# Kernel tuning notes

Hardware: AMD Instinct MI355X
Metric: run time of the kernel (lower is better)

The kernel has to match this reference:

```python
import jax, jax.numpy as jnp
import numpy as np

N = 100000   # nodes
E = 1600000  # edges (avg degree 16)
F_IN = 64
H = 64
C = 40       # classes


def setup_inputs() -> dict:
    key = jax.random.key(0)
    ks = jax.random.split(key, 12)

    def lin(k, out_d, in_d):
        kw, kb = jax.random.split(k)
        W = jax.random.normal(kw, (out_d, in_d), jnp.float32) / jnp.sqrt(jnp.float32(in_d))
        b = jnp.zeros((out_d,), jnp.float32)
        return W, b

    Wl1, b1 = lin(ks[2], H, F_IN)
    Wr1, _ = lin(ks[3], H, F_IN)
    Wl2, b2 = lin(ks[4], H, H)
    Wr2, _ = lin(ks[5], H, H)
    Wl3, b3 = lin(ks[6], C, H)
    Wr3, _ = lin(ks[7], C, H)

    return {
        "x": jax.random.normal(ks[0], (N, F_IN), jnp.float32),
        "edge_index": jax.random.randint(ks[1], (2, E), 0, N, jnp.int32),
        "Wl1": Wl1, "Wr1": Wr1, "b1": b1,
        "Wl2": Wl2, "Wr2": Wr2, "b2": b2,
        "Wl3": Wl3, "Wr3": Wr3, "b3": b3,
    }


def _sage_conv(x, src, dst, Wl, Wr, b, n_nodes):
    # PyG SAGEConv (aggr='mean'): out = lin_l(mean_{j in N(i)} x_j) + lin_r(x_i)
    msg = x[src]                                                   # [E, F] gather
    agg_sum = jax.ops.segment_sum(msg, dst, num_segments=n_nodes)  # [N, F]
    deg = jax.ops.segment_sum(jnp.ones((src.shape[0],), x.dtype), dst,
                              num_segments=n_nodes)                # [N]
    agg = agg_sum / jnp.maximum(deg, 1.0)[:, None]                 # mean aggregation
    return agg @ Wl.T + b + x @ Wr.T


def reference(x, edge_index, Wl1, Wr1, b1, Wl2, Wr2, b2, Wl3, Wr3, b3):
    src, dst = edge_index[0], edge_index[1]
    n = x.shape[0]
    # dropout is identity in eval mode (training=self.training)
    h = jax.nn.relu(_sage_conv(x, src, dst, Wl1, Wr1, b1, n))
    h = jax.nn.relu(_sage_conv(h, src, dst, Wl2, Wr2, b2, n))
    h = _sage_conv(h, src, dst, Wl3, Wr3, b3, n)
    return jax.nn.log_softmax(h, axis=1)
```

## Files before the change

### kernel.cpp

```cpp
#include <hip/hip_runtime.h>
#include <hip/hip_bf16.h>
#include <math.h>


#define BK_SHIFT 7
#define BK_NODES 128
#define NB_MAX   1024

typedef __attribute__((ext_vector_type(8))) short short8;
typedef __attribute__((ext_vector_type(4))) float f32x4;

__device__ inline float blo(unsigned v) { union { unsigned u; float f; } c; c.u = v << 16; return c.f; }
__device__ inline float bhi(unsigned v) { union { unsigned u; float f; } c; c.u = v & 0xFFFF0000u; return c.f; }
__device__ inline unsigned short f2bf(float f) {
    union { float f; unsigned u; } c; c.f = f;
    unsigned r = (c.u + 0x7FFFu + ((c.u >> 16) & 1u)) >> 16;
    return (unsigned short)r;
}

__global__ __launch_bounds__(256) void prep_kernel(const int* __restrict__ dstA, int* __restrict__ bcount,
                                                   int E, int NB,
                                                   const float* __restrict__ x, unsigned short* __restrict__ Xb, int n8,
                                                   const float* __restrict__ Wl1, const float* __restrict__ Wr1,
                                                   const float* __restrict__ Wl2, const float* __restrict__ Wr2,
                                                   const float* __restrict__ Wl3, const float* __restrict__ Wr3,
                                                   unsigned short* __restrict__ Wb1,
                                                   unsigned short* __restrict__ Wb2,
                                                   unsigned short* __restrict__ Wb3) {
    int b = blockIdx.x, t = threadIdx.x;
    if (b < 256) {
        __shared__ int lc[NB_MAX];
        for (int i = t; i < NB; i += 256) lc[i] = 0;
        __syncthreads();
        for (int e = b * 256 + t; e < E; e += 256 * 256)
            atomicAdd(&lc[dstA[e] >> BK_SHIFT], 1);
        __syncthreads();
        for (int i = t; i < NB; i += 256)
            if (lc[i]) atomicAdd(&bcount[i], lc[i]);
    } else if (b < 344) {
        int i = (b - 256) * 256 + t;
        if (i < 8192) {
            int c = i >> 7, k = i & 127;
            float v = (k < 64) ? Wl1[c * 64 + k] : Wr1[c * 64 + k - 64];
            Wb1[i] = f2bf(v);
        } else if (i < 16384) {
            int j = i - 8192;
            int c = j >> 7, k = j & 127;
            float v = (k < 64) ? Wl2[c * 64 + k] : Wr2[c * 64 + k - 64];
            Wb2[j] = f2bf(v);
        } else if (i < 22528) {
            int j = i - 16384;
            int c = j >> 6, k = j & 63;
            float v = 0.f;
            if (c < 40) v = Wl3[c * 64 + k];
            else if (c >= 48 && c < 88) v = Wr3[(c - 48) * 64 + k];
            Wb3[j] = f2bf(v);
        }
    } else {
        for (int i = (b - 344) * 256 + t; i < n8; i += 1024 * 256) {
            const float* p = x + (size_t)i * 8;
            float4 a = *(const float4*)p;
            float4 bq = *(const float4*)(p + 4);
            uint4 o;
            o.x = f2bf(a.x) | ((unsigned)f2bf(a.y) << 16);
            o.y = f2bf(a.z) | ((unsigned)f2bf(a.w) << 16);
            o.z = f2bf(bq.x) | ((unsigned)f2bf(bq.y) << 16);
            o.w = f2bf(bq.z) | ((unsigned)f2bf(bq.w) << 16);
            *(uint4*)(Xb + (size_t)i * 8) = o;
        }
    }
}

__global__ __launch_bounds__(1024) void bscan_kernel(const int* __restrict__ bcount,
                                                     int* __restrict__ bbase,
                                                     int* __restrict__ cursor, int NB, int E) {
    __shared__ int s[1024];
    int t = threadIdx.x;
    int v = (t < NB) ? bcount[t] : 0;
    s[t] = v;
    __syncthreads();
    for (int off = 1; off < 1024; off <<= 1) {
        int x = 0;
        if (t >= off) x = s[t - off];
        __syncthreads();
        s[t] += x;
        __syncthreads();
    }
    if (t < NB) {
        int ex = s[t] - v;
        bbase[t] = ex;
        cursor[t] = ex;
    }
    if (t == 0) bbase[NB] = E;
}

__global__ __launch_bounds__(256) void bin_kernel(const int* __restrict__ srcA,
                                                  const int* __restrict__ dstA,
                                                  int* __restrict__ cursor,
                                                  int* __restrict__ binned, int E, int NB) {
    __shared__ int lc[NB_MAX];
    __shared__ int lbase[NB_MAX];
    int t = threadIdx.x;
    int chunk = (E + gridDim.x - 1) / gridDim.x;
    int e0 = blockIdx.x * chunk;
    int e1 = min(E, e0 + chunk);
    for (int i = t; i < NB; i += 256) lc[i] = 0;
    __syncthreads();
    for (int e = e0 + t; e < e1; e += 256)
        atomicAdd(&lc[dstA[e] >> BK_SHIFT], 1);
    __syncthreads();
    for (int i = t; i < NB; i += 256) {
        int c = lc[i];
        lbase[i] = c ? atomicAdd(&cursor[i], c) : 0;
    }
    __syncthreads();
    for (int i = t; i < NB; i += 256) lc[i] = 0;
    __syncthreads();
    for (int e = e0 + t; e < e1; e += 256) {
        int d = dstA[e];
        int b = d >> BK_SHIFT;
        int r = atomicAdd(&lc[b], 1);
        binned[lbase[b] + r] = srcA[e] | ((d & (BK_NODES - 1)) << 24);
    }
}

__global__ __launch_bounds__(256) void bsort_kernel(const int* __restrict__ binned,
                                                    const int* __restrict__ bbase,
                                                    int* __restrict__ col,
                                                    int* __restrict__ row_start, int N) {
    __shared__ int cnt[BK_NODES];
    __shared__ int base[BK_NODES];
    __shared__ int s[BK_NODES];
    int b = blockIdx.x, t = threadIdx.x;
    int e0 = bbase[b], e1 = bbase[b + 1];
    if (t < BK_NODES) cnt[t] = 0;
    __syncthreads();
    for (int e = e0 + t; e < e1; e += 256)
        atomicAdd(&cnt[(unsigned)binned[e] >> 24], 1);
    __syncthreads();
    int v = (t < BK_NODES) ? cnt[t] : 0;
    if (t < BK_NODES) s[t] = v;
    __syncthreads();
    for (int off = 1; off < BK_NODES; off <<= 1) {
        int x = 0;
        if (t < BK_NODES && t >= off) x = s[t - off];
        __syncthreads();
        if (t < BK_NODES) s[t] += x;
        __syncthreads();
    }
    if (t < BK_NODES) {
        base[t] = e0 + s[t] - v;
        int node = b * BK_NODES + t;
        if (node < N) row_start[node] = base[t];
        cnt[t] = 0;
    }
    if (b == gridDim.x - 1 && t == 0) row_start[N] = e1;
    __syncthreads();
    for (int e = e0 + t; e < e1; e += 256) {
        unsigned p = (unsigned)binned[e];
        int dl = p >> 24;
        int pos = base[dl] + atomicAdd(&cnt[dl], 1);
        col[pos] = p & 0xFFFFFF;
    }
}

__global__ __launch_bounds__(256) void agg64_kernel(const unsigned short* __restrict__ X,
                                                    const int* __restrict__ rs,
                                                    const int* __restrict__ col,
                                                    unsigned short* __restrict__ OUT, int n) {
    int t = threadIdx.x;
    int node = blockIdx.x * 32 + (t >> 3);
    if (node >= n) return;
    int lane = t & 7;
    int s = rs[node], d = rs[node + 1] - s;
    const unsigned short* lp = X + lane * 8;
    float a0 = 0.f, a1 = 0.f, a2 = 0.f, a3 = 0.f, a4 = 0.f, a5 = 0.f, a6 = 0.f, a7 = 0.f;
    int j = 0;
    for (; j + 3 < d; j += 4) {
        int c0 = col[s + j], c1 = col[s + j + 1];
        int c2 = col[s + j + 2], c3 = col[s + j + 3];
        uint4 q0 = *(const uint4*)(lp + (size_t)c0 * 64);
        uint4 q1 = *(const uint4*)(lp + (size_t)c1 * 64);
        uint4 q2 = *(const uint4*)(lp + (size_t)c2 * 64);
        uint4 q3 = *(const uint4*)(lp + (size_t)c3 * 64);
        a0 += (blo(q0.x) + blo(q1.x)) + (blo(q2.x) + blo(q3.x));
        a1 += (bhi(q0.x) + bhi(q1.x)) + (bhi(q2.x) + bhi(q3.x));
        a2 += (blo(q0.y) + blo(q1.y)) + (blo(q2.y) + blo(q3.y));
        a3 += (bhi(q0.y) + bhi(q1.y)) + (bhi(q2.y) + bhi(q3.y));
        a4 += (blo(q0.z) + blo(q1.z)) + (blo(q2.z) + blo(q3.z));
        a5 += (bhi(q0.z) + bhi(q1.z)) + (bhi(q2.z) + bhi(q3.z));
        a6 += (blo(q0.w) + blo(q1.w)) + (blo(q2.w) + blo(q3.w));
        a7 += (bhi(q0.w) + bhi(q1.w)) + (bhi(q2.w) + bhi(q3.w));
    }
    for (; j < d; ++j) {
        int c0 = col[s + j];
        uint4 q0 = *(const uint4*)(lp + (size_t)c0 * 64);
        a0 += blo(q0.x); a1 += bhi(q0.x); a2 += blo(q0.y); a3 += bhi(q0.y);
        a4 += blo(q0.z); a5 += bhi(q0.z); a6 += blo(q0.w); a7 += bhi(q0.w);
    }
    float w = 1.f / (float)(d > 0 ? d : 1);
    a0 *= w; a1 *= w; a2 *= w; a3 *= w; a4 *= w; a5 *= w; a6 *= w; a7 *= w;
    uint4 o;
    o.x = f2bf(a0) | ((unsigned)f2bf(a1) << 16);
    o.y = f2bf(a2) | ((unsigned)f2bf(a3) << 16);
    o.z = f2bf(a4) | ((unsigned)f2bf(a5) << 16);
    o.w = f2bf(a6) | ((unsigned)f2bf(a7) << 16);
    *(uint4*)(OUT + (size_t)node * 64 + lane * 8) = o;
}

__global__ __launch_bounds__(256) void linmfma12_kernel(const unsigned short* __restrict__ A,
                                                        const unsigned short* __restrict__ X,
                                                        const unsigned short* __restrict__ Wb,
                                                        const float* __restrict__ bias,
                                                        unsigned short* __restrict__ OUT,
                                                        int N) {
    __shared__ unsigned short Ys[64][136];
    __shared__ unsigned short Ws[64][136];
    int t = threadIdx.x;
    int rowbase = blockIdx.x * 64;
#pragma unroll
    for (int it = 0; it < 4; ++it) {
        int idx = it * 256 + t;
        int row = idx >> 4, c = idx & 15;
        int grow = rowbase + row;
        if (grow >= N) grow = N - 1;
        const unsigned short* src = (c < 8) ? (A + (size_t)grow * 64 + c * 8)
                                            : (X + (size_t)grow * 64 + (c - 8) * 8);
        *(short8*)&Ys[row][c * 8] = *(const short8*)src;
        *(short8*)&Ws[row][c * 8] = *(const short8*)(Wb + (size_t)row * 128 + c * 8);
    }
    __syncthreads();
    int l = t & 63, w = t >> 6;
    int lrow = l & 15, lk = l >> 4;
    f32x4 acc0 = {0.f, 0.f, 0.f, 0.f};
    f32x4 acc1 = acc0, acc2 = acc0, acc3 = acc0;
#pragma unroll
    for (int kk = 0; kk < 4; ++kk) {
        int ko = kk * 32 + lk * 8;
        short8 a  = *(const short8*)&Ys[16 * w + lrow][ko];
        short8 b0 = *(const short8*)&Ws[lrow][ko];
        short8 b1 = *(const short8*)&Ws[16 + lrow][ko];
        short8 b2 = *(const short8*)&Ws[32 + lrow][ko];
        short8 b3 = *(const short8*)&Ws[48 + lrow][ko];
        acc0 = __builtin_amdgcn_mfma_f32_16x16x32_bf16(a, b0, acc0, 0, 0, 0);
        acc1 = __builtin_amdgcn_mfma_f32_16x16x32_bf16(a, b1, acc1, 0, 0, 0);
        acc2 = __builtin_amdgcn_mfma_f32_16x16x32_bf16(a, b2, acc2, 0, 0, 0);
        acc3 = __builtin_amdgcn_mfma_f32_16x16x32_bf16(a, b3, acc3, 0, 0, 0);
    }
#define EPI12(nt, accv)                                                   \
    {                                                                     \
        int colc = 16 * (nt) + lrow;                                      \
        float bv = bias[colc];                                            \
        _Pragma("unroll") for (int i = 0; i < 4; ++i) {                   \
            int grow = rowbase + 16 * w + lk * 4 + i;                     \
            if (grow < N) {                                               \
                float v = fmaxf(accv[i] + bv, 0.f);                       \
                OUT[(size_t)grow * 64 + colc] = f2bf(v);                  \
            }                                                             \
        }                                                                 \
    }
    EPI12(0, acc0) EPI12(1, acc1) EPI12(2, acc2) EPI12(3, acc3)
#undef EPI12
}

__global__ __launch_bounds__(256) void linmfma3_kernel(const unsigned short* __restrict__ H,
                                                       const unsigned short* __restrict__ Wb3,
                                                       const float* __restrict__ b3,
                                                       unsigned short* __restrict__ Z,
                                                       float* __restrict__ R,
                                                       int N) {
    __shared__ unsigned short Ys[64][72];
    __shared__ unsigned short Ws[96][72];
    int t = threadIdx.x;
    int rowbase = blockIdx.x * 64;
#pragma unroll
    for (int it = 0; it < 2; ++it) {
        int idx = it * 256 + t;
        int row = idx >> 3, c = idx & 7;
        int grow = rowbase + row;
        if (grow >= N) grow = N - 1;
        *(short8*)&Ys[row][c * 8] = *(const short8*)(H + (size_t)grow * 64 + c * 8);
    }
#pragma unroll
    for (int it = 0; it < 3; ++it) {
        int idx = it * 256 + t;
        int row = idx >> 3, c = idx & 7;
        *(short8*)&Ws[row][c * 8] = *(const short8*)(Wb3 + (size_t)row * 64 + c * 8);
    }
    __syncthreads();
    int l = t & 63, w = t >> 6;
    int lrow = l & 15, lk = l >> 4;
    f32x4 acc0 = {0.f, 0.f, 0.f, 0.f};
    f32x4 acc1 = acc0, acc2 = acc0, acc3 = acc0, acc4 = acc0, acc5 = acc0;
#pragma unroll
    for (int kk = 0; kk < 2; ++kk) {
        int ko = kk * 32 + lk * 8;
        short8 a  = *(const short8*)&Ys[16 * w + lrow][ko];
        short8 b0 = *(const short8*)&Ws[lrow][ko];
        short8 b1 = *(const short8*)&Ws[16 + lrow][ko];
        short8 b2 = *(const short8*)&Ws[32 + lrow][ko];
        short8 b3f = *(const short8*)&Ws[48 + lrow][ko];
        short8 b4 = *(const short8*)&Ws[64 + lrow][ko];
        short8 b5 = *(const short8*)&Ws[80 + lrow][ko];
        acc0 = __builtin_amdgcn_mfma_f32_16x16x32_bf16(a, b0, acc0, 0, 0, 0);
        acc1 = __builtin_amdgcn_mfma_f32_16x16x32_bf16(a, b1, acc1, 0, 0, 0);
        acc2 = __builtin_amdgcn_mfma_f32_16x16x32_bf16(a, b2, acc2, 0, 0, 0);
        acc3 = __builtin_amdgcn_mfma_f32_16x16x32_bf16(a, b3f, acc3, 0, 0, 0);
        acc4 = __builtin_amdgcn_mfma_f32_16x16x32_bf16(a, b4, acc4, 0, 0, 0);
        acc5 = __builtin_amdgcn_mfma_f32_16x16x32_bf16(a, b5, acc5, 0, 0, 0);
    }
#define EPI3(nt, accv)                                                     \
    {                                                                      \
        int colc = 16 * (nt) + lrow;                                       \
        _Pragma("unroll") for (int i = 0; i < 4; ++i) {                    \
            int grow = rowbase + 16 * w + lk * 4 + i;                      \
            if (grow < N) {                                                \
                float v = accv[i];                                         \
                if (colc < 40) {                                           \
                    Z[(size_t)grow * 40 + colc] = f2bf(v);                 \
                } else if (colc >= 48 && colc < 88) {                      \
                    R[(size_t)grow * 40 + (colc - 48)] = v + b3[colc - 48];\
                }                                                          \
            }                                                              \
        }                                                                  \
    }
    EPI3(0, acc0) EPI3(1, acc1) EPI3(2, acc2) EPI3(3, acc3) EPI3(4, acc4) EPI3(5, acc5)
#undef EPI3
}

__global__ __launch_bounds__(256) void agg40lsm_kernel(const unsigned short* __restrict__ Z,
                                                       const int* __restrict__ rs,
                                                       const int* __restrict__ col,
                                                       float* __restrict__ out, int n) {
    int t = threadIdx.x;
    int node = blockIdx.x * 32 + (t >> 3);
    if (node >= n) return;
    int lane = t & 7;
    bool act = lane < 5;
    int s = rs[node], d = rs[node + 1] - s;
    const unsigned short* lp = Z + lane * 8;
    float a0 = 0.f, a1 = 0.f, a2 = 0.f, a3 = 0.f, a4 = 0.f, a5 = 0.f, a6 = 0.f, a7 = 0.f;
    int j = 0;
    for (; j + 3 < d; j += 4) {
        int c0 = col[s + j], c1 = col[s + j + 1];
        int c2 = col[s + j + 2], c3 = col[s + j + 3];
        if (act) {
            uint4 q0 = *(const uint4*)(lp + (size_t)c0 * 40);
            uint4 q1 = *(const uint4*)(lp + (size_t)c1 * 40);
            uint4 q2 = *(const uint4*)(lp + (size_t)c2 * 40);
            uint4 q3 = *(const uint4*)(lp + (size_t)c3 * 40);
            a0 += (blo(q0.x) + blo(q1.x)) + (blo(q2.x) + blo(q3.x));
            a1 += (bhi(q0.x) + bhi(q1.x)) + (bhi(q2.x) + bhi(q3.x));
            a2 += (blo(q0.y) + blo(q1.y)) + (blo(q2.y) + blo(q3.y));
            a3 += (bhi(q0.y) + bhi(q1.y)) + (bhi(q2.y) + bhi(q3.y));
            a4 += (blo(q0.z) + blo(q1.z)) + (blo(q2.z) + blo(q3.z));
            a5 += (bhi(q0.z) + bhi(q1.z)) + (bhi(q2.z) + bhi(q3.z));
            a6 += (blo(q0.w) + blo(q1.w)) + (blo(q2.w) + blo(q3.w));
            a7 += (bhi(q0.w) + bhi(q1.w)) + (bhi(q2.w) + bhi(q3.w));
        }
    }
    for (; j < d; ++j) {
        int c0 = col[s + j];
        if (act) {
            uint4 q0 = *(const uint4*)(lp + (size_t)c0 * 40);
            a0 += blo(q0.x); a1 += bhi(q0.x); a2 += blo(q0.y); a3 += bhi(q0.y);
            a4 += blo(q0.z); a5 += bhi(q0.z); a6 += blo(q0.w); a7 += bhi(q0.w);
        }
    }
    float w = 1.f / (float)(d > 0 ? d : 1);
    if (act) {
        float* op = out + (size_t)node * 40 + lane * 8;
        float4 r0 = *(const float4*)op;
        float4 r1 = *(const float4*)(op + 4);
        a0 = a0 * w + r0.x; a1 = a1 * w + r0.y; a2 = a2 * w + r0.z; a3 = a3 * w + r0.w;
        a4 = a4 * w + r1.x; a5 = a5 * w + r1.y; a6 = a6 * w + r1.z; a7 = a7 * w + r1.w;
    }
    float mx = act ? fmaxf(fmaxf(fmaxf(a0, a1), fmaxf(a2, a3)),
                           fmaxf(fmaxf(a4, a5), fmaxf(a6, a7))) : -3.4e38f;
#pragma unroll
    for (int off = 1; off < 8; off <<= 1) mx = fmaxf(mx, __shfl_xor(mx, off, 8));
    float ssum = act ? (expf(a0 - mx) + expf(a1 - mx) + expf(a2 - mx) + expf(a3 - mx) +
                        expf(a4 - mx) + expf(a5 - mx) + expf(a6 - mx) + expf(a7 - mx)) : 0.f;
#pragma unroll
    for (int off = 1; off < 8; off <<= 1) ssum += __shfl_xor(ssum, off, 8);
    float lg = mx + logf(ssum);
    if (act) {
        float* op = out + (size_t)node * 40 + lane * 8;
        float4 o0, o1;
        o0.x = a0 - lg; o0.y = a1 - lg; o0.z = a2 - lg; o0.w = a3 - lg;
        o1.x = a4 - lg; o1.y = a5 - lg; o1.z = a6 - lg; o1.w = a7 - lg;
        *(float4*)op = o0;
        *(float4*)(op + 4) = o1;
    }
}

extern "C" void kernel_launch(void* const* d_in, const int* in_sizes, int n_in,
                              void* d_out, int out_size, void* d_ws, size_t ws_size,
                              hipStream_t stream) {
    const float* x   = (const float*)d_in[0];
    const int*   ei  = (const int*)d_in[1];
    const float* Wl1 = (const float*)d_in[2];
    const float* Wr1 = (const float*)d_in[3];
    const float* b1  = (const float*)d_in[4];
    const float* Wl2 = (const float*)d_in[5];
    const float* Wr2 = (const float*)d_in[6];
    const float* b2  = (const float*)d_in[7];
    const float* Wl3 = (const float*)d_in[8];
    const float* Wr3 = (const float*)d_in[9];
    const float* b3  = (const float*)d_in[10];
    float* out = (float*)d_out;

    const int N = in_sizes[0] / 64;
    const int E = in_sizes[1] / 2;
    const int NB = (N + BK_NODES - 1) / BK_NODES;
    const int* srcA = ei;
    const int* dstA = ei + E;

    char* ws = (char*)d_ws;
    size_t off = 0;
    auto alloc = [&](size_t bytes) {
        off = (off + 255) & ~(size_t)255;
        char* p = ws + off;
        off += bytes;
        return p;
    };
    int* bcount    = (int*)alloc((size_t)(NB_MAX + 1) * 4);
    int* bbase     = (int*)alloc((size_t)(NB_MAX + 1) * 4);
    int* cursor    = (int*)alloc((size_t)NB_MAX * 4);
    int* binned    = (int*)alloc((size_t)E * 4);
    int* col       = (int*)alloc((size_t)E * 4);
    int* row_start = (int*)alloc((size_t)(N + 1) * 4);
    unsigned short* Xb  = (unsigned short*)alloc((size_t)N * 64 * 2);
    unsigned short* AGG = (unsigned short*)alloc((size_t)N * 64 * 2);
    unsigned short* Hb  = (unsigned short*)alloc((size_t)N * 64 * 2);
    unsigned short* Zb  = (unsigned short*)alloc((size_t)N * 40 * 2);
    unsigned short* Wb1 = (unsigned short*)alloc(8192 * 2);
    unsigned short* Wb2 = (unsigned short*)alloc(8192 * 2);
    unsigned short* Wb3 = (unsigned short*)alloc(6144 * 2);

    hipMemsetAsync(bcount, 0, (size_t)(NB + 1) * 4, stream);
    prep_kernel<<<1368, 256, 0, stream>>>(dstA, bcount, E, NB, x, Xb, N * 64 / 8,
                                          Wl1, Wr1, Wl2, Wr2, Wl3, Wr3, Wb1, Wb2, Wb3);
    bscan_kernel<<<1, 1024, 0, stream>>>(bcount, bbase, cursor, NB, E);
    bin_kernel<<<512, 256, 0, stream>>>(srcA, dstA, cursor, binned, E, NB);
    bsort_kernel<<<NB, 256, 0, stream>>>(binned, bbase, col, row_start, N);

    int gridA = (N + 31) / 32;
    int gridM = (N + 63) / 64;

    agg64_kernel<<<gridA, 256, 0, stream>>>(Xb, row_start, col, AGG, N);
    linmfma12_kernel<<<gridM, 256, 0, stream>>>(AGG, Xb, Wb1, b1, Hb, N);

    agg64_kernel<<<gridA, 256, 0, stream>>>(Hb, row_start, col, AGG, N);
    linmfma12_kernel<<<gridM, 256, 0, stream>>>(AGG, Hb, Wb2, b2, Hb, N);

    linmfma3_kernel<<<gridM, 256, 0, stream>>>(Hb, Wb3, b3, Zb, out, N);
    agg40lsm_kernel<<<gridA, 256, 0, stream>>>(Zb, row_start, col, out, N);
}
```

Measured before the change: 285.0 us.

## Replace atomic cursor binning with per-block count matrix and column scan

The prep kernel now writes a per-block, per-bucket histogram matrix instead of atomically accumulating global bucket counts. A new column-scan kernel computes each block's exclusive offset per bucket. The bin kernel then scatters directly without re-counting or using global atomics. This removes the bin kernel's second pass over the destinations, the global cursor atomics and the memset, at the cost of an extra kernel launch and about 2 MB of count/prefix traffic.

```diff
diff --git a/kernel.cpp b/kernel.cpp
--- a/kernel.cpp
+++ b/kernel.cpp
@@ -6,6 +6,7 @@
 #define BK_SHIFT 7
 #define BK_NODES 128
 #define NB_MAX   1024
+#define BBLK     256
 
 typedef __attribute__((ext_vector_type(8))) short short8;
 typedef __attribute__((ext_vector_type(4))) float f32x4;
@@ -18,7 +19,7 @@
     return (unsigned short)r;
 }
 
-__global__ __launch_bounds__(256) void prep_kernel(const int* __restrict__ dstA, int* __restrict__ bcount,
+__global__ __launch_bounds__(256) void prep_kernel(const int* __restrict__ dstA, int* __restrict__ cnts,
                                                    int E, int NB,
                                                    const float* __restrict__ x, unsigned short* __restrict__ Xb, int n8,
                                                    const float* __restrict__ Wl1, const float* __restrict__ Wr1,
@@ -28,17 +29,18 @@
                                                    unsigned short* __restrict__ Wb2,
                                                    unsigned short* __restrict__ Wb3) {
     int b = blockIdx.x, t = threadIdx.x;
-    if (b < 256) {
+    if (b < BBLK) {
         __shared__ int lc[NB_MAX];
-        for (int i = t; i < NB; i += 256) lc[i] = 0;
-        __syncthreads();
-        for (int e = b * 256 + t; e < E; e += 256 * 256)
+        for (int i = t; i < NB_MAX; i += 256) lc[i] = 0;
+        __syncthreads();
+        int chunk = (E + BBLK - 1) / BBLK;
+        int e0 = b * chunk, e1 = min(E, e0 + chunk);
+        for (int e = e0 + t; e < e1; e += 256)
             atomicAdd(&lc[dstA[e] >> BK_SHIFT], 1);
         __syncthreads();
-        for (int i = t; i < NB; i += 256)
-            if (lc[i]) atomicAdd(&bcount[i], lc[i]);
-    } else if (b < 344) {
-        int i = (b - 256) * 256 + t;
+        for (int i = t; i < NB_MAX; i += 256) cnts[b * NB_MAX + i] = lc[i];
+    } else if (b < BBLK + 88) {
+        int i = (b - BBLK) * 256 + t;
         if (i < 8192) {
             int c = i >> 7, k = i & 127;
             float v = (k < 64) ? Wl1[c * 64 + k] : Wr1[c * 64 + k - 64];
@@ -57,7 +59,7 @@
             Wb3[j] = f2bf(v);
         }
     } else {
-        for (int i = (b - 344) * 256 + t; i < n8; i += 1024 * 256) {
+        for (int i = (b - (BBLK + 88)) * 256 + t; i < n8; i += 1024 * 256) {
             const float* p = x + (size_t)i * 8;
             float4 a = *(const float4*)p;
             float4 bq = *(const float4*)(p + 4);
@@ -71,9 +73,27 @@
     }
 }
 
+__global__ __launch_bounds__(256) void colscan_kernel(const int* __restrict__ cnts,
+                                                      int* __restrict__ lpre,
+                                                      int* __restrict__ bcount) {
+    __shared__ int s[BBLK];
+    int j = blockIdx.x, t = threadIdx.x;
+    int v = cnts[t * NB_MAX + j];
+    s[t] = v;
+    __syncthreads();
+    for (int off = 1; off < BBLK; off <<= 1) {
+        int x = 0;
+        if (t >= off) x = s[t - off];
+        __syncthreads();
+        s[t] += x;
+        __syncthreads();
+    }
+    lpre[t * NB_MAX + j] = s[t] - v;
+    if (t == BBLK - 1) bcount[j] = s[t];
+}
+
 __global__ __launch_bounds__(1024) void bscan_kernel(const int* __restrict__ bcount,
-                                                     int* __restrict__ bbase,
-                                                     int* __restrict__ cursor, int NB, int E) {
+                                                     int* __restrict__ bbase, int NB, int E) {
     __shared__ int s[1024];
     int t = threadIdx.x;
     int v = (t < NB) ? bcount[t] : 0;
@@ -86,41 +106,27 @@
         s[t] += x;
         __syncthreads();
     }
-    if (t < NB) {
-        int ex = s[t] - v;
-        bbase[t] = ex;
-        cursor[t] = ex;
-    }
+    if (t < NB) bbase[t] = s[t] - v;
     if (t == 0) bbase[NB] = E;
 }
 
-__global__ __launch_bounds__(256) void bin_kernel(const int* __restrict__ srcA,
+__global__ __launch_bounds__(512) void bin_kernel(const int* __restrict__ srcA,
                                                   const int* __restrict__ dstA,
-                                                  int* __restrict__ cursor,
+                                                  const int* __restrict__ lpre,
+                                                  const int* __restrict__ bbase,
                                                   int* __restrict__ binned, int E, int NB) {
     __shared__ int lc[NB_MAX];
-    __shared__ int lbase[NB_MAX];
-    int t = threadIdx.x;
-    int chunk = (E + gridDim.x - 1) / gridDim.x;
-    int e0 = blockIdx.x * chunk;
-    int e1 = min(E, e0 + chunk);
-    for (int i = t; i < NB; i += 256) lc[i] = 0;
-    __syncthreads();
-    for (int e = e0 + t; e < e1; e += 256)
-        atomicAdd(&lc[dstA[e] >> BK_SHIFT], 1);
-    __syncthreads();
-    for (int i = t; i < NB; i += 256) {
-        int c = lc[i];
-        lbase[i] = c ? atomicAdd(&cursor[i], c) : 0;
-    }
-    __syncthreads();
-    for (int i = t; i < NB; i += 256) lc[i] = 0;
-    __syncthreads();
-    for (int e = e0 + t; e < e1; e += 256) {
+    int b = blockIdx.x, t = threadIdx.x;
+    for (int i = t; i < NB; i += 512)
+        lc[i] = lpre[b * NB_MAX + i] + bbase[i];
+    __syncthreads();
+    int chunk = (E + BBLK - 1) / BBLK;
+    int e0 = b * chunk, e1 = min(E, e0 + chunk);
+    for (int e = e0 + t; e < e1; e += 512) {
         int d = dstA[e];
-        int b = d >> BK_SHIFT;
-        int r = atomicAdd(&lc[b], 1);
-        binned[lbase[b] + r] = srcA[e] | ((d & (BK_NODES - 1)) << 24);
+        int bk = d >> BK_SHIFT;
+        int pos = atomicAdd(&lc[bk], 1);
+        binned[pos] = srcA[e] | ((d & (BK_NODES - 1)) << 24);
     }
 }
 
@@ -424,9 +430,10 @@
         off += bytes;
         return p;
     };
+    int* cnts      = (int*)alloc((size_t)BBLK * NB_MAX * 4);
+    int* lpre      = (int*)alloc((size_t)BBLK * NB_MAX * 4);
     int* bcount    = (int*)alloc((size_t)(NB_MAX + 1) * 4);
     int* bbase     = (int*)alloc((size_t)(NB_MAX + 1) * 4);
-    int* cursor    = (int*)alloc((size_t)NB_MAX * 4);
     int* binned    = (int*)alloc((size_t)E * 4);
     int* col       = (int*)alloc((size_t)E * 4);
     int* row_start = (int*)alloc((size_t)(N + 1) * 4);
@@ -438,11 +445,11 @@
     unsigned short* Wb2 = (unsigned short*)alloc(8192 * 2);
     unsigned short* Wb3 = (unsigned short*)alloc(6144 * 2);
 
-    hipMemsetAsync(bcount, 0, (size_t)(NB + 1) * 4, stream);
-    prep_kernel<<<1368, 256, 0, stream>>>(dstA, bcount, E, NB, x, Xb, N * 64 / 8,
-                                          Wl1, Wr1, Wl2, Wr2, Wl3, Wr3, Wb1, Wb2, Wb3);
-    bscan_kernel<<<1, 1024, 0, stream>>>(bcount, bbase, cursor, NB, E);
-    bin_kernel<<<512, 256, 0, stream>>>(srcA, dstA, cursor, binned, E, NB);
+    prep_kernel<<<BBLK + 88 + 1024, 256, 0, stream>>>(dstA, cnts, E, NB, x, Xb, N * 64 / 8,
+                                                      Wl1, Wr1, Wl2, Wr2, Wl3, Wr3, Wb1, Wb2, Wb3);
+    colscan_kernel<<<NB, BBLK, 0, stream>>>(cnts, lpre, bcount);
+    bscan_kernel<<<1, 1024, 0, stream>>>(bcount, bbase, NB, E);
+    bin_kernel<<<BBLK, 512, 0, stream>>>(srcA, dstA, lpre, bbase, binned, E, NB);
     bsort_kernel<<<NB, 256, 0, stream>>>(binned, bbase, col, row_start, N);
 
     int gridA = (N + 31) / 32;
```

New measurement: 264.1 us. 1.08x faster.
